# Kernel optimization log

Measured on AMD Instinct MI355X. Metric: run time of the kernel, lower is better.

Reference implementation:

```python
import jax, jax.numpy as jnp
import numpy as np

C, H, P = 128, 4, 8  # d_model, n_heads, n_points (n_levels=1)
D = C // H


def setup_inputs() -> dict:
    key = jax.random.key(0)
    ks = jax.random.split(key, 14)
    B, Y, X = 2, 200, 200
    N = Y * X
    s = 0.05
    inp = {
        "query": jax.random.normal(ks[0], (B, N, C), jnp.float32),
        "query_pos": jax.random.normal(ks[1], (B, N, C), jnp.float32),
        # MSDeformAttn params
        "Wv": jax.random.normal(ks[2], (C, C), jnp.float32) * s,
        "bv": jnp.zeros((C,), jnp.float32),
        "Woff": jax.random.normal(ks[3], (C, H * P * 2), jnp.float32) * s,
        "boff": jax.random.normal(ks[4], (H * P * 2,), jnp.float32) * s,
        "Wattn": jax.random.normal(ks[5], (C, H * P), jnp.float32) * s,
        "battn": jnp.zeros((H * P,), jnp.float32),
        "Wout1": jax.random.normal(ks[6], (C, C), jnp.float32) * s,  # MSDeformAttn.output_proj
        "bout1": jnp.zeros((C,), jnp.float32),
        "Wout2": jax.random.normal(ks[7], (C, C), jnp.float32) * s,  # wrapper output_proj
        "bout2": jnp.zeros((C,), jnp.float32),
        "Y": Y,
        "X": X,
    }
    return inp


def _deform_attn(q, v_in, Wv, bv, Woff, boff, Wattn, battn, Wout1, bout1, Y, X):
    B, N, _ = q.shape
    # reference points: grid centers, stacked (y, x) normalized (as in source)
    ref_y = (jnp.arange(Y, dtype=jnp.float32) + 0.5) / Y
    ref_x = (jnp.arange(X, dtype=jnp.float32) + 0.5) / X
    ry, rx = jnp.meshgrid(ref_y, ref_x, indexing="ij")
    ref = jnp.stack([ry.reshape(-1), rx.reshape(-1)], -1)  # (N, 2)

    value = (v_in @ Wv + bv).reshape(B, Y, X, H, D).transpose(0, 3, 1, 2, 4)  # (B,H,Y,X,D)
    off = (q @ Woff + boff).reshape(B, N, H, P, 2)
    attn = jax.nn.softmax((q @ Wattn + battn).reshape(B, N, H, P), axis=-1)

    # offset normalizer = (W, H) = (X, Y); loc = ref + off/norm  (faithful to source)
    norm = jnp.array([X, Y], jnp.float32)
    loc = ref[None, :, None, None, :] + off / norm  # (B,N,H,P,2)

    # grid_sample bilinear, align_corners=False, zero padding; channel 0 = x, 1 = y
    gx = loc[..., 0] * X - 0.5
    gy = loc[..., 1] * Y - 0.5
    x0 = jnp.floor(gx)
    y0 = jnp.floor(gy)
    wx1 = gx - x0
    wy1 = gy - y0
    x0i = x0.astype(jnp.int32)
    y0i = y0.astype(jnp.int32)

    b_idx = jnp.arange(B)[:, None, None, None]
    h_idx = jnp.arange(H)[None, None, :, None]

    def gather(yi, xi, w):
        valid = (yi >= 0) & (yi < Y) & (xi >= 0) & (xi < X)
        yc = jnp.clip(yi, 0, Y - 1)
        xc = jnp.clip(xi, 0, X - 1)
        v = value[b_idx, h_idx, yc, xc]  # (B,N,H,P,D)
        return v * (w * valid)[..., None]

    sampled = (
        gather(y0i, x0i, (1 - wy1) * (1 - wx1))
        + gather(y0i, x0i + 1, (1 - wy1) * wx1)
        + gather(y0i + 1, x0i, wy1 * (1 - wx1))
        + gather(y0i + 1, x0i + 1, wy1 * wx1)
    )
    out = (sampled * attn[..., None]).sum(axis=3).reshape(B, N, C)
    return out @ Wout1 + bout1


def reference(query, query_pos, Wv, bv, Woff, boff, Wattn, battn, Wout1, bout1, Wout2, bout2, Y, X):
    residual = query
    q = query + query_pos
    out = _deform_attn(q, q, Wv, bv, Woff, boff, Wattn, battn, Wout1, bout1, Y, X)
    out = out @ Wout2 + bout2  # wrapper output_proj; dropout in eval mode = identity
    return out + residual
```

## Files before the change

kernel.cpp:

```cpp
#include <hip/hip_runtime.h>
#include <hip/hip_bf16.h>
#include <hip/hip_fp16.h>

#define BQ 2
#define YY 200
#define XX 200
#define NQ 40000
#define CC 128
#define MTOT 80000
#define NCOL 224
#define NTILES 5000

typedef __attribute__((ext_vector_type(8))) short short8;
typedef __attribute__((ext_vector_type(4))) short short4v;
typedef __attribute__((ext_vector_type(4))) float f32x4;

static __device__ __forceinline__ unsigned short f2bf(float f) {
    union { float f; unsigned int u; } v; v.f = f;
    unsigned int r = v.u + 0x7FFF + ((v.u >> 16) & 1);
    return (unsigned short)(r >> 16);
}
static __device__ __forceinline__ unsigned short f2bf_hw(float f) {
    __hip_bfloat16 h = __float2bfloat16(f);
    unsigned short s;
    __builtin_memcpy(&s, &h, 2);
    return s;
}
static __device__ __forceinline__ __half2 u2h2(unsigned int u) {
    __half2 h; __builtin_memcpy(&h, &u, 4); return h;
}
static __device__ __forceinline__ unsigned int h22u(__half2 h) {
    unsigned int u; __builtin_memcpy(&u, &h, 4); return u;
}
static __device__ __forceinline__ short h2s(__half h) {
    short s; __builtin_memcpy(&s, &h, 2); return s;
}
static __device__ __forceinline__ unsigned int packh2(float a, float b) {
    return h22u(__floats2half2_rn(a, b));
}

__global__ void prep_kernel(const float* __restrict__ Wv, const float* __restrict__ Woff,
                            const float* __restrict__ Wattn,
                            const float* __restrict__ Wout1, const float* __restrict__ Wout2,
                            const float* __restrict__ bout1, const float* __restrict__ bout2,
                            unsigned short* __restrict__ WcatT,
                            unsigned short* __restrict__ W12T, float* __restrict__ b12) {
    if (blockIdx.x < 112) {
        int idx = blockIdx.x * 256 + threadIdx.x;
        if (idx >= NCOL * CC) return;
        int c = idx >> 7, k = idx & 127;
        float w = (c < 128) ? Wv[k * 128 + c]
                : (c < 192) ? Woff[k * 64 + (c - 128)]
                            : Wattn[k * 32 + (c - 192)];
        WcatT[c * 128 + k] = f2bf(w);
    } else {
        int idx = (blockIdx.x - 112) * 256 + threadIdx.x;
        int c = idx >> 7, k = idx & 127;
        float s = 0.f;
        for (int j = 0; j < 128; ++j) s += Wout1[k * 128 + j] * Wout2[j * 128 + c];
        W12T[c * 128 + k] = f2bf(s);
        if (k == 0) {
            float t = bout2[c];
            for (int j = 0; j < 128; ++j) t += bout1[j] * Wout2[j * 128 + c];
            b12[c] = t;
        }
    }
}

__global__ __launch_bounds__(256) void qsum_kernel(const float* __restrict__ query,
                                                   const float* __restrict__ qpos,
                                                   unsigned short* __restrict__ qbf) {
    const size_t total = (size_t)MTOT * CC / 8;
    for (size_t c = (size_t)blockIdx.x * 256 + threadIdx.x; c < total;
         c += (size_t)gridDim.x * 256) {
        const float4* a = (const float4*)(query + c * 8);
        const float4* b = (const float4*)(qpos + c * 8);
        float4 a0 = a[0], a1 = a[1], b0 = b[0], b1 = b[1];
        short8 w;
        w[0] = (short)f2bf_hw(a0.x + b0.x); w[1] = (short)f2bf_hw(a0.y + b0.y);
        w[2] = (short)f2bf_hw(a0.z + b0.z); w[3] = (short)f2bf_hw(a0.w + b0.w);
        w[4] = (short)f2bf_hw(a1.x + b1.x); w[5] = (short)f2bf_hw(a1.y + b1.y);
        w[6] = (short)f2bf_hw(a1.z + b1.z); w[7] = (short)f2bf_hw(a1.w + b1.w);
        *(short8*)(qbf + c * 8) = w;
    }
}

__global__ __launch_bounds__(256, 2) void g1_kernel(
    const unsigned short* __restrict__ qbf, const unsigned short* __restrict__ WcatT,
    const float* __restrict__ bv, const float* __restrict__ boff, const float* __restrict__ battn,
    unsigned short* __restrict__ value_h, unsigned short* __restrict__ off_h,
    unsigned short* __restrict__ logits_h)
{
    const int tid = threadIdx.x;
    const int group = blockIdx.x >> 8;
    const int gblk = blockIdx.x & 255;
    const int lane = tid & 63;
    const int arow = lane & 15, kq = lane >> 4;
    const int wid = gblk * 4 + (tid >> 6);
    const int tg0 = group * 4;
    const int NT = (group == 3) ? 2 : 4;

    short8 bf[4][4];
#pragma unroll
    for (int t = 0; t < 4; ++t) {
        if (t < NT) {
#pragma unroll
            for (int ks = 0; ks < 4; ++ks)
                bf[t][ks] = *(const short8*)(WcatT + (size_t)((tg0 + t) * 16 + arow) * 128 + ks * 32 + kq * 8);
        }
    }

    f32x4 biasv[4];
#pragma unroll
    for (int t = 0; t < 4; ++t) {
        if (t < NT) {
            const float* bp = (group < 2) ? (bv + (tg0 + t) * 16 + kq * 4)
                            : (group == 2) ? (boff + (tg0 + t - 8) * 16 + kq * 4)
                                           : (battn + (tg0 + t - 12) * 16 + kq * 4);
            float4 b4 = *(const float4*)bp;
            biasv[t] = (f32x4){b4.x, b4.y, b4.z, b4.w};
        }
    }

    for (int tile = wid; tile < NTILES; tile += 1024) {
        const char* pa = (const char*)qbf + (size_t)(tile * 16 + arow) * 256 + kq * 16;
        short8 af[4];
#pragma unroll
        for (int ks = 0; ks < 4; ++ks) af[ks] = *(const short8*)(pa + ks * 64);

        f32x4 acc[4];
#pragma unroll
        for (int t = 0; t < 4; ++t) acc[t] = biasv[t];

#pragma unroll
        for (int ks = 0; ks < 4; ++ks) {
#pragma unroll
            for (int t = 0; t < 4; ++t) {
                if (t < NT)
                    acc[t] = __builtin_amdgcn_mfma_f32_16x16x32_bf16(bf[t][ks], af[ks], acc[t], 0, 0, 0);
            }
        }

        const int row = tile * 16 + arow;
        if (group < 2) {
#pragma unroll
            for (int t = 0; t < 4; ++t) {
                short4v pv;
                pv[0] = h2s(__float2half(acc[t][0])); pv[1] = h2s(__float2half(acc[t][1]));
                pv[2] = h2s(__float2half(acc[t][2])); pv[3] = h2s(__float2half(acc[t][3]));
                *(short4v*)(value_h + (size_t)row * 128 + (tg0 + t) * 16 + kq * 4) = pv;
            }
        } else if (group == 2) {
#pragma unroll
            for (int t = 0; t < 4; ++t) {
                uint2 pk;
                pk.x = packh2(acc[t][0], acc[t][1]);
                pk.y = packh2(acc[t][2], acc[t][3]);
                *(uint2*)(off_h + (size_t)row * 64 + (tg0 + t - 8) * 16 + kq * 4) = pk;
            }
        } else {
#pragma unroll
            for (int t = 0; t < 2; ++t) {
                uint2 pk;
                pk.x = packh2(acc[t][0], acc[t][1]);
                pk.y = packh2(acc[t][2], acc[t][3]);
                *(uint2*)(logits_h + (size_t)row * 32 + (tg0 + t - 12) * 16 + kq * 4) = pk;
            }
        }
    }
}

__global__ __launch_bounds__(512, 2) void sg2_kernel(
    const unsigned short* __restrict__ value_h, const unsigned short* __restrict__ off_h,
    const unsigned short* __restrict__ logits_h, const unsigned short* __restrict__ W12T,
    const float* __restrict__ b12, const float* __restrict__ query, float* __restrict__ out)
{
    __shared__ int4 SA[16][36];
    __shared__ int4 SW[16][36];
    __shared__ unsigned char Stile[16 * 272];

    const int tid = threadIdx.x;
    const int qi = tid >> 5;
    const int lane = tid & 31;
    const int r = blockIdx.x * 16 + qi;
    const int b = (r >= NQ) ? 1 : 0;
    const int n = r - b * NQ;
    const int yq = n / XX, xq = n - yq * XX;

    {
        float lg = __half2float(*(const __half*)(logits_h + (size_t)r * 32 + lane));
        float m = lg;
        m = fmaxf(m, __shfl_xor(m, 1));
        m = fmaxf(m, __shfl_xor(m, 2));
        m = fmaxf(m, __shfl_xor(m, 4));
        float e = __expf(lg - m);
        float s = e;
        s += __shfl_xor(s, 1);
        s += __shfl_xor(s, 2);
        s += __shfl_xor(s, 4);
        float aw = e / s;

        __half2 oh = u2h2(*(const unsigned int*)(off_h + (size_t)r * 64 + lane * 2));
        float gx = (float)yq + __low2float(oh);
        float gy = (float)xq + __high2float(oh);
        float fx = floorf(gx), fy = floorf(gy);
        int x0 = (int)fx, y0 = (int)fy;
        float wx1 = gx - fx, wy1 = gy - fy;
        float vx0 = ((unsigned)x0 < XX) ? 1.f : 0.f;
        float vx1 = ((unsigned)(x0 + 1) < XX) ? 1.f : 0.f;
        float vy0 = ((unsigned)y0 < YY) ? 1.f : 0.f;
        float vy1 = ((unsigned)(y0 + 1) < YY) ? 1.f : 0.f;
        int x0c = min(max(x0, 0), XX - 1);
        int x1c = min(max(x0 + 1, 0), XX - 1);
        int y0c = min(max(y0, 0), YY - 1);
        int y1c = min(max(y0 + 1, 0), YY - 1);
        int hb = (lane >> 3) * 64;
        int rowA = y0c * XX, rowB = y1c * XX;
        int4 addrs;
        addrs.x = (rowA + x0c) * 256 + hb;
        addrs.y = (rowA + x1c) * 256 + hb;
        addrs.z = (rowB + x0c) * 256 + hb;
        addrs.w = (rowB + x1c) * 256 + hb;

        float wxa = (1.f - wx1) * vx0;
        float wxb = wx1 * vx1;
        float wya = aw * (1.f - wy1) * vy0;
        float wyb = aw * wy1 * vy1;
        int4 wts;
        wts.x = (int)h22u(__float2half2_rn(wxa * wya));
        wts.y = (int)h22u(__float2half2_rn(wxb * wya));
        wts.z = (int)h22u(__float2half2_rn(wxa * wyb));
        wts.w = (int)h22u(__float2half2_rn(wxb * wyb));

        const int slot = (lane & 7) * 4 + (lane >> 3);
        SA[qi][slot] = addrs;
        SW[qi][slot] = wts;
    }
    __syncthreads();

    {
        const char* vb = (const char*)(value_h + (size_t)b * NQ * 128);
        const int h = lane >> 3, yc = (lane >> 2) & 1, quad = lane & 3;
        const int cb = quad * 16;

        int2 a[8];
#pragma unroll
        for (int p = 0; p < 8; ++p)
            a[p] = *(const int2*)((const char*)&SA[qi][p * 4 + h] + yc * 8);

        uint4 d0[8], d1[8];
#pragma unroll
        for (int p = 0; p < 8; ++p) {
            d0[p] = *(const uint4*)(vb + a[p].x + cb);
            d1[p] = *(const uint4*)(vb + a[p].y + cb);
        }
        __builtin_amdgcn_sched_barrier(0);

        int2 w[8];
#pragma unroll
        for (int p = 0; p < 8; ++p)
            w[p] = *(const int2*)((const char*)&SW[qi][p * 4 + h] + yc * 8);

        __half2 acc0 = __float2half2_rn(0.f), acc1 = __float2half2_rn(0.f);
        __half2 acc2 = __float2half2_rn(0.f), acc3 = __float2half2_rn(0.f);

#pragma unroll
        for (int p = 0; p < 8; ++p) {
            __half2 wa = u2h2((unsigned int)w[p].x);
            __half2 wb = u2h2((unsigned int)w[p].y);
            acc0 = __hfma2(wa, u2h2(d0[p].x), acc0);
            acc1 = __hfma2(wa, u2h2(d0[p].y), acc1);
            acc2 = __hfma2(wa, u2h2(d0[p].z), acc2);
            acc3 = __hfma2(wa, u2h2(d0[p].w), acc3);
            acc0 = __hfma2(wb, u2h2(d1[p].x), acc0);
            acc1 = __hfma2(wb, u2h2(d1[p].y), acc1);
            acc2 = __hfma2(wb, u2h2(d1[p].z), acc2);
            acc3 = __hfma2(wb, u2h2(d1[p].w), acc3);
        }

        acc0 = __hadd2(acc0, u2h2((unsigned int)__shfl_xor((int)h22u(acc0), 4)));
        acc1 = __hadd2(acc1, u2h2((unsigned int)__shfl_xor((int)h22u(acc1), 4)));
        acc2 = __hadd2(acc2, u2h2((unsigned int)__shfl_xor((int)h22u(acc2), 4)));
        acc3 = __hadd2(acc3, u2h2((unsigned int)__shfl_xor((int)h22u(acc3), 4)));

        __half2 pa = (yc == 0) ? acc0 : acc2;
        __half2 pb = (yc == 0) ? acc1 : acc3;
        uint2 packed;
        packed.x = ((unsigned int)f2bf(__high2float(pa)) << 16) | (unsigned int)f2bf(__low2float(pa));
        packed.y = ((unsigned int)f2bf(__high2float(pb)) << 16) | (unsigned int)f2bf(__low2float(pb));
        *(uint2*)(Stile + qi * 272 + h * 64 + cb + yc * 8) = packed;
    }
    __syncthreads();

    {
        const int w = tid >> 6;
        const int lane64 = tid & 63;
        const int arow = lane64 & 15, kq = lane64 >> 4;
        const int qbase = blockIdx.x * 16;

        short8 bfr[4];
#pragma unroll
        for (int ks = 0; ks < 4; ++ks)
            bfr[ks] = *(const short8*)(W12T + (size_t)(w * 16 + arow) * 128 + ks * 32 + kq * 8);

        float4 b4 = *(const float4*)(b12 + w * 16 + kq * 4);
        f32x4 acc = (f32x4){b4.x, b4.y, b4.z, b4.w};

        short8 af[4];
#pragma unroll
        for (int ks = 0; ks < 4; ++ks)
            af[ks] = *(const short8*)(Stile + arow * 272 + ks * 64 + kq * 16);

#pragma unroll
        for (int ks = 0; ks < 4; ++ks)
            acc = __builtin_amdgcn_mfma_f32_16x16x32_bf16(bfr[ks], af[ks], acc, 0, 0, 0);

        size_t idx = (size_t)(qbase + arow) * 128 + w * 16 + kq * 4;
        float4 q4 = *(const float4*)(query + idx);
        float4 o = make_float4(acc[0] + q4.x, acc[1] + q4.y, acc[2] + q4.z, acc[3] + q4.w);
        *(float4*)(out + idx) = o;
    }
}

extern "C" void kernel_launch(void* const* d_in, const int* in_sizes, int n_in,
                              void* d_out, int out_size, void* d_ws, size_t ws_size,
                              hipStream_t stream) {
    const float* query = (const float*)d_in[0];
    const float* qpos  = (const float*)d_in[1];
    const float* Wv    = (const float*)d_in[2];
    const float* bv    = (const float*)d_in[3];
    const float* Woff  = (const float*)d_in[4];
    const float* boff  = (const float*)d_in[5];
    const float* Wattn = (const float*)d_in[6];
    const float* battn = (const float*)d_in[7];
    const float* Wout1 = (const float*)d_in[8];
    const float* bout1 = (const float*)d_in[9];
    const float* Wout2 = (const float*)d_in[10];
    const float* bout2 = (const float*)d_in[11];
    float* out = (float*)d_out;

    char* ws = (char*)d_ws;
    unsigned short* value_h  = (unsigned short*)(ws);
    unsigned short* off_h    = (unsigned short*)(ws + 20480000);
    unsigned short* logits_h = (unsigned short*)(ws + 40960000);
    unsigned short* qbf      = (unsigned short*)(ws + 51200000);
    unsigned short* WcatT    = (unsigned short*)(ws + 71680000);
    unsigned short* W12T     = (unsigned short*)(ws + 71680000 + 57344);
    float*          b12      = (float*)(ws + 71680000 + 57344 + 32768);

    prep_kernel<<<176, 256, 0, stream>>>(Wv, Woff, Wattn, Wout1, Wout2, bout1, bout2,
                                         WcatT, W12T, b12);
    qsum_kernel<<<2048, 256, 0, stream>>>(query, qpos, qbf);
    g1_kernel<<<1024, 256, 0, stream>>>(qbf, WcatT, bv, boff, battn,
                                        value_h, off_h, logits_h);
    sg2_kernel<<<NTILES, 512, 0, stream>>>(value_h, off_h, logits_h, W12T, b12, query, out);
}
```

Before: 102.2 us.

## Use a full 64-lane wavefront per query in the sampling kernel

The sampling kernel moves from 32 lanes per query (512-thread blocks) to a full 64-lane wavefront per query (1024-thread blocks). Each lane now gathers one bilinear corner with one 16-byte load instead of two, which halves per-lane gather registers and exposes more memory parallelism. An extra shuffle-xor stage reduces across corners. The cost is that half the lanes idle during the softmax/address phase and half the waves idle during the MFMA projection phase, and the larger blocks may lower occupancy.

```diff
diff --git a/kernel.cpp b/kernel.cpp
--- a/kernel.cpp
+++ b/kernel.cpp
@@ -14,6 +14,7 @@
 typedef __attribute__((ext_vector_type(8))) short short8;
 typedef __attribute__((ext_vector_type(4))) short short4v;
 typedef __attribute__((ext_vector_type(4))) float f32x4;
+typedef __attribute__((ext_vector_type(4))) unsigned int u32x4;
 
 static __device__ __forceinline__ unsigned short f2bf(float f) {
     union { float f; unsigned int u; } v; v.f = f;
@@ -170,7 +171,7 @@
     }
 }
 
-__global__ __launch_bounds__(512, 2) void sg2_kernel(
+__global__ __launch_bounds__(1024, 4) void sg2_kernel(
     const unsigned short* __restrict__ value_h, const unsigned short* __restrict__ off_h,
     const unsigned short* __restrict__ logits_h, const unsigned short* __restrict__ W12T,
     const float* __restrict__ b12, const float* __restrict__ query, float* __restrict__ out)
@@ -180,15 +181,17 @@
     __shared__ unsigned char Stile[16 * 272];
 
     const int tid = threadIdx.x;
-    const int qi = tid >> 5;
-    const int lane = tid & 31;
+    const int qi = tid >> 6;
+    const int lane = tid & 63;
     const int r = blockIdx.x * 16 + qi;
     const int b = (r >= NQ) ? 1 : 0;
-    const int n = r - b * NQ;
-    const int yq = n / XX, xq = n - yq * XX;
-
-    {
-        float lg = __half2float(*(const __half*)(logits_h + (size_t)r * 32 + lane));
+
+    if (lane < 32) {
+        const int lane32 = lane;
+        const int n = r - b * NQ;
+        const int yq = n / XX, xq = n - yq * XX;
+
+        float lg = __half2float(*(const __half*)(logits_h + (size_t)r * 32 + lane32));
         float m = lg;
         m = fmaxf(m, __shfl_xor(m, 1));
         m = fmaxf(m, __shfl_xor(m, 2));
@@ -200,7 +203,7 @@
         s += __shfl_xor(s, 4);
         float aw = e / s;
 
-        __half2 oh = u2h2(*(const unsigned int*)(off_h + (size_t)r * 64 + lane * 2));
+        __half2 oh = u2h2(*(const unsigned int*)(off_h + (size_t)r * 64 + lane32 * 2));
         float gx = (float)yq + __low2float(oh);
         float gy = (float)xq + __high2float(oh);
         float fx = floorf(gx), fy = floorf(gy);
@@ -214,7 +217,7 @@
         int x1c = min(max(x0 + 1, 0), XX - 1);
         int y0c = min(max(y0, 0), YY - 1);
         int y1c = min(max(y0 + 1, 0), YY - 1);
-        int hb = (lane >> 3) * 64;
+        int hb = (lane32 >> 3) * 64;
         int rowA = y0c * XX, rowB = y1c * XX;
         int4 addrs;
         addrs.x = (rowA + x0c) * 256 + hb;
@@ -232,7 +235,7 @@
         wts.z = (int)h22u(__float2half2_rn(wxa * wyb));
         wts.w = (int)h22u(__float2half2_rn(wxb * wyb));
 
-        const int slot = (lane & 7) * 4 + (lane >> 3);
+        const int slot = (lane32 & 7) * 4 + (lane32 >> 3);
         SA[qi][slot] = addrs;
         SW[qi][slot] = wts;
     }
@@ -240,62 +243,66 @@
 
     {
         const char* vb = (const char*)(value_h + (size_t)b * NQ * 128);
-        const int h = lane >> 3, yc = (lane >> 2) & 1, quad = lane & 3;
-        const int cb = quad * 16;
-
-        int2 a[8];
+        const int h = lane >> 4;
+        const int cidx = (lane >> 2) & 3;
+        const int quad = lane & 3;
+
+        int av[8], wv[8];
+#pragma unroll
+        for (int p = 0; p < 8; ++p) {
+            av[p] = ((const int*)&SA[qi][p * 4 + h])[cidx];
+            wv[p] = ((const int*)&SW[qi][p * 4 + h])[cidx];
+        }
+
+        u32x4 d[8];
 #pragma unroll
         for (int p = 0; p < 8; ++p)
-            a[p] = *(const int2*)((const char*)&SA[qi][p * 4 + h] + yc * 8);
-
-        uint4 d0[8], d1[8];
+            d[p] = *(const u32x4*)(vb + av[p] + quad * 16);
+        __builtin_amdgcn_sched_barrier(0);
+
+        __half2 aA0 = __float2half2_rn(0.f), aA1 = aA0, aA2 = aA0, aA3 = aA0;
+        __half2 aB0 = aA0, aB1 = aA0, aB2 = aA0, aB3 = aA0;
 #pragma unroll
         for (int p = 0; p < 8; ++p) {
-            d0[p] = *(const uint4*)(vb + a[p].x + cb);
-            d1[p] = *(const uint4*)(vb + a[p].y + cb);
-        }
-        __builtin_amdgcn_sched_barrier(0);
-
-        int2 w[8];
-#pragma unroll
-        for (int p = 0; p < 8; ++p)
-            w[p] = *(const int2*)((const char*)&SW[qi][p * 4 + h] + yc * 8);
-
-        __half2 acc0 = __float2half2_rn(0.f), acc1 = __float2half2_rn(0.f);
-        __half2 acc2 = __float2half2_rn(0.f), acc3 = __float2half2_rn(0.f);
-
-#pragma unroll
-        for (int p = 0; p < 8; ++p) {
-            __half2 wa = u2h2((unsigned int)w[p].x);
-            __half2 wb = u2h2((unsigned int)w[p].y);
-            acc0 = __hfma2(wa, u2h2(d0[p].x), acc0);
-            acc1 = __hfma2(wa, u2h2(d0[p].y), acc1);
-            acc2 = __hfma2(wa, u2h2(d0[p].z), acc2);
-            acc3 = __hfma2(wa, u2h2(d0[p].w), acc3);
-            acc0 = __hfma2(wb, u2h2(d1[p].x), acc0);
-            acc1 = __hfma2(wb, u2h2(d1[p].y), acc1);
-            acc2 = __hfma2(wb, u2h2(d1[p].z), acc2);
-            acc3 = __hfma2(wb, u2h2(d1[p].w), acc3);
-        }
-
-        acc0 = __hadd2(acc0, u2h2((unsigned int)__shfl_xor((int)h22u(acc0), 4)));
-        acc1 = __hadd2(acc1, u2h2((unsigned int)__shfl_xor((int)h22u(acc1), 4)));
-        acc2 = __hadd2(acc2, u2h2((unsigned int)__shfl_xor((int)h22u(acc2), 4)));
-        acc3 = __hadd2(acc3, u2h2((unsigned int)__shfl_xor((int)h22u(acc3), 4)));
-
-        __half2 pa = (yc == 0) ? acc0 : acc2;
-        __half2 pb = (yc == 0) ? acc1 : acc3;
-        uint2 packed;
-        packed.x = ((unsigned int)f2bf(__high2float(pa)) << 16) | (unsigned int)f2bf(__low2float(pa));
-        packed.y = ((unsigned int)f2bf(__high2float(pb)) << 16) | (unsigned int)f2bf(__low2float(pb));
-        *(uint2*)(Stile + qi * 272 + h * 64 + cb + yc * 8) = packed;
+            __half2 w2 = u2h2((unsigned int)wv[p]);
+            if ((p & 1) == 0) {
+                aA0 = __hfma2(w2, u2h2(d[p][0]), aA0);
+                aA1 = __hfma2(w2, u2h2(d[p][1]), aA1);
+                aA2 = __hfma2(w2, u2h2(d[p][2]), aA2);
+                aA3 = __hfma2(w2, u2h2(d[p][3]), aA3);
+            } else {
+                aB0 = __hfma2(w2, u2h2(d[p][0]), aB0);
+                aB1 = __hfma2(w2, u2h2(d[p][1]), aB1);
+                aB2 = __hfma2(w2, u2h2(d[p][2]), aB2);
+                aB3 = __hfma2(w2, u2h2(d[p][3]), aB3);
+            }
+        }
+        __half2 a0 = __hadd2(aA0, aB0), a1 = __hadd2(aA1, aB1);
+        __half2 a2 = __hadd2(aA2, aB2), a3 = __hadd2(aA3, aB3);
+
+        a0 = __hadd2(a0, u2h2((unsigned int)__shfl_xor((int)h22u(a0), 4)));
+        a1 = __hadd2(a1, u2h2((unsigned int)__shfl_xor((int)h22u(a1), 4)));
+        a2 = __hadd2(a2, u2h2((unsigned int)__shfl_xor((int)h22u(a2), 4)));
+        a3 = __hadd2(a3, u2h2((unsigned int)__shfl_xor((int)h22u(a3), 4)));
+        a0 = __hadd2(a0, u2h2((unsigned int)__shfl_xor((int)h22u(a0), 8)));
+        a1 = __hadd2(a1, u2h2((unsigned int)__shfl_xor((int)h22u(a1), 8)));
+        a2 = __hadd2(a2, u2h2((unsigned int)__shfl_xor((int)h22u(a2), 8)));
+        a3 = __hadd2(a3, u2h2((unsigned int)__shfl_xor((int)h22u(a3), 8)));
+
+        if (cidx == 0) {
+            u32x4 pk;
+            pk[0] = ((unsigned int)f2bf(__high2float(a0)) << 16) | (unsigned int)f2bf(__low2float(a0));
+            pk[1] = ((unsigned int)f2bf(__high2float(a1)) << 16) | (unsigned int)f2bf(__low2float(a1));
+            pk[2] = ((unsigned int)f2bf(__high2float(a2)) << 16) | (unsigned int)f2bf(__low2float(a2));
+            pk[3] = ((unsigned int)f2bf(__high2float(a3)) << 16) | (unsigned int)f2bf(__low2float(a3));
+            *(u32x4*)(Stile + qi * 272 + h * 64 + quad * 16) = pk;
+        }
     }
     __syncthreads();
 
-    {
-        const int w = tid >> 6;
-        const int lane64 = tid & 63;
-        const int arow = lane64 & 15, kq = lane64 >> 4;
+    if (qi < 8) {
+        const int w = qi;
+        const int arow = lane & 15, kq = lane >> 4;
         const int qbase = blockIdx.x * 16;
 
         short8 bfr[4];
@@ -353,5 +360,5 @@
     qsum_kernel<<<2048, 256, 0, stream>>>(query, qpos, qbf);
     g1_kernel<<<1024, 256, 0, stream>>>(qbf, WcatT, bv, boff, battn,
                                         value_h, off_h, logits_h);
-    sg2_kernel<<<NTILES, 512, 0, stream>>>(value_h, off_h, logits_h, W12T, b12, query, out);
-}
+    sg2_kernel<<<NTILES, 1024, 0, stream>>>(value_h, off_h, logits_h, W12T, b12, query, out);
+}
```

After: 111.4 us. 1.09x slower.
